# Kernel tuning notes

Hardware: AMD Instinct MI355X
Metric: run time of the kernel (lower is better)

## Reference

```python
import jax, jax.numpy as jnp
import numpy as np

N = 40000
E = 640000
D_IN = 128
D_HID = 128
N_CLS = 40


def setup_inputs() -> dict:
    key = jax.random.key(0)
    ks = jax.random.split(key, 12)
    x = jax.random.normal(ks[0], (N, D_IN), dtype=jnp.float32)
    edge_index = jax.random.randint(ks[1], (2, E), 0, N, dtype=jnp.int32)
    s = 1.0 / np.sqrt(D_IN)
    sh = 1.0 / np.sqrt(D_HID)
    sc = 1.0 / np.sqrt(4 * D_HID)
    # per-layer params: lin weight [out,in], combine weight [out, 4*out], bias [out]
    W0 = jax.random.uniform(ks[2], (D_HID, D_IN), jnp.float32, -s, s)
    C0 = jax.random.uniform(ks[3], (D_HID, 4 * D_HID), jnp.float32, -sc, sc)
    b0 = jnp.zeros((D_HID,), jnp.float32)
    W1 = jax.random.uniform(ks[4], (D_HID, D_HID), jnp.float32, -sh, sh)
    C1 = jax.random.uniform(ks[5], (D_HID, 4 * D_HID), jnp.float32, -sc, sc)
    b1 = jnp.zeros((D_HID,), jnp.float32)
    Wout = jax.random.uniform(ks[6], (N_CLS, D_HID), jnp.float32, -sh, sh)
    bout = jax.random.uniform(ks[7], (N_CLS,), jnp.float32, -sh, sh)
    return {"x": x, "edge_index": edge_index, "W0": W0, "C0": C0, "b0": b0,
            "W1": W1, "C1": C1, "b1": b1, "Wout": Wout, "bout": bout}


def _gcn_layer(x, row, col, W, C, b):
    n = x.shape[0]
    h = x @ W.T  # [N, H]
    ones = jnp.ones(row.shape, x.dtype)
    deg = jax.ops.segment_sum(ones, col, num_segments=n)  # in-degree incl. self-loops
    dinv = jnp.where(deg > 0, deg ** -0.5, 0.0)
    norm = dinv[row] * dinv[col]  # [E]
    msg = norm[:, None] * h[row]  # gather + scale, [E, H]
    add = jax.ops.segment_sum(msg, col, num_segments=n)
    mean = add / jnp.maximum(deg, 1.0)[:, None]
    mn = jax.ops.segment_min(msg, col, num_segments=n)
    mx = jax.ops.segment_max(msg, col, num_segments=n)
    out = jnp.concatenate([mean, add, mn, mx], axis=-1) @ C.T  # [N, H]
    return out + b


def reference(x, edge_index, W0, C0, b0, W1, C1, b1, Wout, bout):
    n = x.shape[0]
    loops = jnp.arange(n, dtype=edge_index.dtype)
    row = jnp.concatenate([edge_index[0], loops])
    col = jnp.concatenate([edge_index[1], loops])
    h = jax.nn.relu(_gcn_layer(x, row, col, W0, C0, b0))
    h = jax.nn.relu(_gcn_layer(h, row, col, W1, C1, b1))
    logits = h @ Wout.T + bout
    return jax.nn.log_softmax(logits, axis=-1)
```

## Files before the change

kernel.cpp:

```cpp
#include <hip/hip_runtime.h>
#include <hip/hip_fp16.h>
#include <math.h>

#define NN 40000
#define NE 640000
#define D 128
#define NCLS 40
#define CAP 64

typedef _Float16 f16x8 __attribute__((ext_vector_type(8)));
typedef float    f32x4 __attribute__((ext_vector_type(4)));

static inline int cdiv(int a, int b){ return (a + b - 1) / b; }

__global__ __launch_bounds__(256) void k_prep(int* __restrict__ cnt,
    const float* __restrict__ W0, _Float16* __restrict__ w0h,
    const float* __restrict__ C0, _Float16* __restrict__ c0h,
    const float* __restrict__ W1, _Float16* __restrict__ w1h,
    const float* __restrict__ C1, _Float16* __restrict__ c1h,
    const float* __restrict__ WO, _Float16* __restrict__ oh) {
  int i = blockIdx.x * 256 + threadIdx.x;
  if (i < NN) cnt[i] = 0;
  if (i < 16384) {
    float v = W0[i];
    int cc = i >> 7, k = i & 127;
    int pidx = (((cc >> 4) * 4 + (k >> 5)) * 64 + ((cc & 15) | (((k >> 3) & 3) << 4))) * 8 + (k & 7);
    w0h[pidx] = (_Float16)v;
  } else if (i < 81920) {
    int off = i - 16384;
    c0h[off] = (_Float16)C0[off];
  } else if (i < 98304) {
    int off = i - 81920;
    w1h[off] = (_Float16)W1[off];
  } else if (i < 163840) {
    int off = i - 98304;
    c1h[off] = (_Float16)C1[off];
  } else if (i < 168960) {
    int off = i - 163840;
    oh[off] = (_Float16)WO[off];
  }
}

__global__ __launch_bounds__(256) void k_fill(const int* __restrict__ row,
                                              const int* __restrict__ col,
                                              int* __restrict__ cnt,
                                              int* __restrict__ adj) {
  int i = blockIdx.x * 256 + threadIdx.x;
  if (i < NE) {
    int c = col[i];
    int s = atomicAdd(&cnt[c], 1);
    if (s < CAP) adj[c * CAP + s] = row[i];
  }
}

__global__ __launch_bounds__(256) void k_dinvlin(const int* __restrict__ cnt,
                                                 float* __restrict__ dinv,
                                                 const float* __restrict__ A,
                                                 const _Float16* __restrict__ Wh,
                                                 _Float16* __restrict__ out) {
  if (blockIdx.x < 157) {
    int i = blockIdx.x * 256 + threadIdx.x;
    if (i < NN) dinv[i] = rsqrtf((float)(cnt[i] + 1));
    return;
  }
  __shared__ f16x8 Ah[64 * 8];
  int t = threadIdx.x;
  int lane = t & 63, wid = t >> 6;
  int wr = wid >> 1, wc = wid & 1;
  int row0 = (blockIdx.x - 157) * 64;

  f32x4 acc[2][4];
  #pragma unroll
  for (int m = 0; m < 2; m++)
    #pragma unroll
    for (int n = 0; n < 4; n++) acc[m][n] = (f32x4){0.f, 0.f, 0.f, 0.f};

  for (int k0 = 0; k0 < 128; k0 += 64) {
    __syncthreads();
    #pragma unroll
    for (int c = 0; c < 2; c++) {
      int id = t + c * 256;
      int r = id >> 3, q = id & 7;
      int ch = r * 8 + (q ^ (r & 7));
      const float* src = &A[(size_t)(row0 + r) * 128 + k0 + q * 8];
      float4 v0 = *(const float4*)src;
      float4 v1 = *(const float4*)(src + 4);
      float vv[8] = {v0.x, v0.y, v0.z, v0.w, v1.x, v1.y, v1.z, v1.w};
      f16x8 hi;
      #pragma unroll
      for (int j = 0; j < 8; j++) hi[j] = (_Float16)vv[j];
      Ah[ch] = hi;
    }
    __syncthreads();
    #pragma unroll
    for (int ks = 0; ks < 2; ks++) {
      int kchunk = (k0 >> 5) + ks;
      f16x8 ah[2], bh[4];
      #pragma unroll
      for (int m = 0; m < 2; m++) {
        int row = wr * 32 + m * 16 + (lane & 15);
        int ch = row * 8 + ((ks * 4 + (lane >> 4)) ^ (row & 7));
        ah[m] = Ah[ch];
      }
      #pragma unroll
      for (int n = 0; n < 4; n++) {
        int fidx = (((wc * 4 + n) * 4 + kchunk) * 64 + lane) * 8;
        bh[n] = *(const f16x8*)&Wh[fidx];
      }
      #pragma unroll
      for (int m = 0; m < 2; m++)
        #pragma unroll
        for (int n = 0; n < 4; n++)
          acc[m][n] = __builtin_amdgcn_mfma_f32_16x16x32_f16(ah[m], bh[n], acc[m][n], 0, 0, 0);
    }
  }

  #pragma unroll
  for (int m = 0; m < 2; m++) {
    int rbase = row0 + wr * 32 + m * 16 + (lane >> 4) * 4;
    float rs[4];
    #pragma unroll
    for (int j = 0; j < 4; j++) rs[j] = rsqrtf((float)(cnt[rbase + j] + 1));
    #pragma unroll
    for (int n = 0; n < 4; n++) {
      int col = wc * 64 + n * 16 + (lane & 15);
      #pragma unroll
      for (int j = 0; j < 4; j++)
        out[(size_t)(rbase + j) * 128 + col] = (_Float16)(acc[m][n][j] * rs[j]);
    }
  }
}

__global__ __launch_bounds__(256) void k_agg(const _Float16* __restrict__ hs,
                                             const int* __restrict__ cnt,
                                             const int* __restrict__ adj,
                                             const float* __restrict__ dinv,
                                             _Float16* __restrict__ agg) {
  int t = threadIdx.x;
  int g = t >> 4;
  int sl = t & 15;
  int nd = blockIdx.x * 16 + g;
  float di = dinv[nd];
  f16x8 sum = *(const f16x8*)&hs[(size_t)nd * D + sl * 8];
  f16x8 mn = sum, mx = sum;
  int ec = cnt[nd]; if (ec > CAP) ec = CAP;
  const int* abase = &adj[(size_t)nd * CAP];

  for (int eb = 0; eb < ec; eb += 16) {
    int rem = ec - eb; if (rem > 16) rem = 16;
    int re = abase[eb + (sl < rem ? sl : rem - 1)];
    int j = 0;
    for (; j + 8 <= rem; j += 8) {
      int r[8]; f16x8 v[8];
      #pragma unroll
      for (int u = 0; u < 8; u++) r[u] = __shfl(re, j + u, 16);
      #pragma unroll
      for (int u = 0; u < 8; u++) v[u] = *(const f16x8*)&hs[(size_t)r[u] * D + sl * 8];
      #pragma unroll
      for (int u = 0; u < 8; u++) {
        sum += v[u];
        mn = __builtin_elementwise_min(mn, v[u]);
        mx = __builtin_elementwise_max(mx, v[u]);
      }
    }
    for (; j + 4 <= rem; j += 4) {
      int r[4]; f16x8 v[4];
      #pragma unroll
      for (int u = 0; u < 4; u++) r[u] = __shfl(re, j + u, 16);
      #pragma unroll
      for (int u = 0; u < 4; u++) v[u] = *(const f16x8*)&hs[(size_t)r[u] * D + sl * 8];
      #pragma unroll
      for (int u = 0; u < 4; u++) {
        sum += v[u];
        mn = __builtin_elementwise_min(mn, v[u]);
        mx = __builtin_elementwise_max(mx, v[u]);
      }
    }
    for (; j < rem; j++) {
      int r0 = __shfl(re, j, 16);
      f16x8 v0 = *(const f16x8*)&hs[(size_t)r0 * D + sl * 8];
      sum += v0;
      mn = __builtin_elementwise_min(mn, v0);
      mx = __builtin_elementwise_max(mx, v0);
    }
  }

  _Float16 dh = (_Float16)di;
  f16x8 dv = {dh, dh, dh, dh, dh, dh, dh, dh};
  size_t base = (size_t)nd * 384 + sl * 8;
  *(f16x8*)&agg[base +   0] = sum * dv;
  *(f16x8*)&agg[base + 128] = mn  * dv;
  *(f16x8*)&agg[base + 256] = mx  * dv;
}

template<int MODE>
__global__ __launch_bounds__(256, 4) void k_comb(const _Float16* __restrict__ agg,
                                                 const float* __restrict__ dinv,
                                                 const _Float16* __restrict__ CW,
                                                 const float* __restrict__ bias,
                                                 const _Float16* __restrict__ W2h,
                                                 const float* __restrict__ bias2,
                                                 void* __restrict__ outv) {
  __shared__ f16x8 As[32 * 48];
  __shared__ f16x8 Bs[128 * 8];
  int t = threadIdx.x;
  int lane = t & 63, wid = t >> 6;
  int nd0 = blockIdx.x * 32;

  #pragma unroll
  for (int c = 0; c < 6; c++) {
    int id = t + c * 256;
    int r = id / 48, q = id - r * 48;
    As[r * 48 + (q ^ (r & 7))] = *(const f16x8*)&agg[(size_t)(nd0 + r) * 384 + q * 8];
  }

  f32x4 accA[2][2], accM[2][2];
  #pragma unroll
  for (int m = 0; m < 2; m++)
    #pragma unroll
    for (int n = 0; n < 2; n++) {
      accA[m][n] = (f32x4){0.f, 0.f, 0.f, 0.f};
      accM[m][n] = (f32x4){0.f, 0.f, 0.f, 0.f};
    }

  for (int k0 = 0; k0 < 512; k0 += 64) {
    __syncthreads();
    #pragma unroll
    for (int c = 0; c < 4; c++) {
      int id = t + c * 256;
      int cc = id >> 3, kq = id & 7;
      Bs[cc * 8 + (kq ^ (cc & 7))] = *(const f16x8*)&CW[(size_t)cc * 512 + k0 + kq * 8];
    }
    __syncthreads();
    int qbase = ((k0 < 256) ? (k0 & 127) : (k0 - 128)) >> 3;
    bool isMean = (k0 < 128);
    #pragma unroll
    for (int ks = 0; ks < 2; ks++) {
      f16x8 a[2], b[2];
      #pragma unroll
      for (int m = 0; m < 2; m++) {
        int row = m * 16 + (lane & 15);
        int qq = qbase + ks * 4 + (lane >> 4);
        a[m] = As[row * 48 + (qq ^ (row & 7))];
      }
      #pragma unroll
      for (int n = 0; n < 2; n++) {
        int cc = wid * 32 + n * 16 + (lane & 15);
        b[n] = Bs[cc * 8 + ((ks * 4 + (lane >> 4)) ^ (cc & 7))];
      }
      #pragma unroll
      for (int m = 0; m < 2; m++)
        #pragma unroll
        for (int n = 0; n < 2; n++) {
          if (isMean)
            accM[m][n] = __builtin_amdgcn_mfma_f32_16x16x32_f16(a[m], b[n], accM[m][n], 0, 0, 0);
          else
            accA[m][n] = __builtin_amdgcn_mfma_f32_16x16x32_f16(a[m], b[n], accA[m][n], 0, 0, 0);
        }
    }
  }

  __syncthreads();
  _Float16* A2 = (_Float16*)As;
  #pragma unroll
  for (int m = 0; m < 2; m++) {
    int lr0 = m * 16 + (lane >> 4) * 4;
    float d2[4];
    #pragma unroll
    for (int j = 0; j < 4; j++) {
      float dvv = dinv[nd0 + lr0 + j];
      d2[j] = dvv * dvv;
    }
    #pragma unroll
    for (int n = 0; n < 2; n++) {
      int cc = wid * 32 + n * 16 + (lane & 15);
      float bv = bias[cc];
      #pragma unroll
      for (int j = 0; j < 4; j++) {
        float v = fmaxf(accA[m][n][j] + d2[j] * accM[m][n][j] + bv, 0.f);
        int r = lr0 + j;
        A2[(r * 48 + 32 + ((cc >> 3) ^ (r & 7))) * 8 + (cc & 7)] = (_Float16)v;
      }
    }
  }

  if constexpr (MODE == 0) {
    f32x4 acc2[2][2];
    #pragma unroll
    for (int m = 0; m < 2; m++)
      #pragma unroll
      for (int n = 0; n < 2; n++) acc2[m][n] = (f32x4){0.f, 0.f, 0.f, 0.f};
    for (int k0 = 0; k0 < 128; k0 += 64) {
      __syncthreads();
      #pragma unroll
      for (int c = 0; c < 4; c++) {
        int id = t + c * 256;
        int cc = id >> 3, kq = id & 7;
        Bs[cc * 8 + (kq ^ (cc & 7))] = *(const f16x8*)&W2h[(size_t)cc * 128 + k0 + kq * 8];
      }
      __syncthreads();
      #pragma unroll
      for (int ks = 0; ks < 2; ks++) {
        int qq = (k0 >> 3) + ks * 4 + (lane >> 4);
        f16x8 a[2], b[2];
        #pragma unroll
        for (int m = 0; m < 2; m++) {
          int row = m * 16 + (lane & 15);
          a[m] = As[row * 48 + 32 + (qq ^ (row & 7))];
        }
        #pragma unroll
        for (int n = 0; n < 2; n++) {
          int cc = wid * 32 + n * 16 + (lane & 15);
          b[n] = Bs[cc * 8 + ((ks * 4 + (lane >> 4)) ^ (cc & 7))];
        }
        #pragma unroll
        for (int m = 0; m < 2; m++)
          #pragma unroll
          for (int n = 0; n < 2; n++)
            acc2[m][n] = __builtin_amdgcn_mfma_f32_16x16x32_f16(a[m], b[n], acc2[m][n], 0, 0, 0);
      }
    }
    _Float16* out = (_Float16*)outv;
    #pragma unroll
    for (int m = 0; m < 2; m++) {
      int rbase = nd0 + m * 16 + (lane >> 4) * 4;
      float rs[4];
      #pragma unroll
      for (int j = 0; j < 4; j++) rs[j] = dinv[rbase + j];
      #pragma unroll
      for (int n = 0; n < 2; n++) {
        int cc = wid * 32 + n * 16 + (lane & 15);
        #pragma unroll
        for (int j = 0; j < 4; j++)
          out[(size_t)(rbase + j) * 128 + cc] = (_Float16)(acc2[m][n][j] * rs[j]);
      }
    }
  } else {
    f32x4 acc3[3];
    #pragma unroll
    for (int n = 0; n < 3; n++) acc3[n] = (f32x4){0.f, 0.f, 0.f, 0.f};
    __syncthreads();
    #pragma unroll
    for (int c = 0; c < 3; c++) {
      int id = t + c * 256;
      int r = id >> 4, q = id & 15;
      f16x8 hv = {};
      if (r < NCLS) hv = *(const f16x8*)&W2h[(size_t)r * 128 + q * 8];
      Bs[r * 16 + (q ^ (r & 15))] = hv;
    }
    __syncthreads();
    if (wid < 2) {
      #pragma unroll
      for (int ks = 0; ks < 4; ks++) {
        int arow = wid * 16 + (lane & 15);
        f16x8 a = As[arow * 48 + 32 + ((ks * 4 + (lane >> 4)) ^ (arow & 7))];
        #pragma unroll
        for (int n = 0; n < 3; n++) {
          int br = n * 16 + (lane & 15);
          f16x8 b = Bs[br * 16 + ((ks * 4 + (lane >> 4)) ^ (br & 15))];
          acc3[n] = __builtin_amdgcn_mfma_f32_16x16x32_f16(a, b, acc3[n], 0, 0, 0);
        }
      }
      float* out = (float*)outv;
      int cl = lane & 15;
      float bb[3];
      #pragma unroll
      for (int n = 0; n < 3; n++) {
        int c = n * 16 + cl;
        bb[n] = (c < NCLS) ? bias2[c] : 0.f;
      }
      #pragma unroll
      for (int j = 0; j < 4; j++) {
        float v[3];
        #pragma unroll
        for (int n = 0; n < 3; n++) {
          int c = n * 16 + cl;
          v[n] = (c < NCLS) ? acc3[n][j] + bb[n] : -INFINITY;
        }
        float m = fmaxf(fmaxf(v[0], v[1]), v[2]);
        #pragma unroll
        for (int off = 1; off < 16; off <<= 1) m = fmaxf(m, __shfl_xor(m, off, 16));
        float s = 0.f;
        #pragma unroll
        for (int n = 0; n < 3; n++) {
          int c = n * 16 + cl;
          if (c < NCLS) s += expf(v[n] - m);
        }
        #pragma unroll
        for (int off = 1; off < 16; off <<= 1) s += __shfl_xor(s, off, 16);
        float ls = logf(s);
        int row = nd0 + wid * 16 + (lane >> 4) * 4 + j;
        #pragma unroll
        for (int n = 0; n < 3; n++) {
          int c = n * 16 + cl;
          if (c < NCLS) out[(size_t)row * NCLS + c] = v[n] - m - ls;
        }
      }
    }
  }
}

extern "C" void kernel_launch(void* const* d_in, const int* in_sizes, int n_in,
                              void* d_out, int out_size, void* d_ws, size_t ws_size,
                              hipStream_t stream) {
  const float* x    = (const float*)d_in[0];
  const int*   ei   = (const int*)  d_in[1];
  const float* W0   = (const float*)d_in[2];
  const float* C0   = (const float*)d_in[3];
  const float* b0   = (const float*)d_in[4];
  const float* W1   = (const float*)d_in[5];
  const float* C1   = (const float*)d_in[6];
  const float* b1   = (const float*)d_in[7];
  const float* Wout = (const float*)d_in[8];
  const float* bout = (const float*)d_in[9];
  float* out = (float*)d_out;

  char* ws = (char*)d_ws;
  size_t o = 0;
  auto take = [&](size_t bytes) -> char* {
    char* p = ws + o;
    o += (bytes + 255) & ~(size_t)255;
    return p;
  };
  int*       cnt    = (int*)      take((size_t)NN * 4);
  int*       adj    = (int*)      take((size_t)NN * CAP * 4);
  float*     dinv   = (float*)    take((size_t)NN * 4);
  _Float16*  W0h    = (_Float16*) take(128 * 128 * 2);
  _Float16*  C0h    = (_Float16*) take(128 * 512 * 2);
  _Float16*  W1h    = (_Float16*) take(128 * 128 * 2);
  _Float16*  C1h    = (_Float16*) take(128 * 512 * 2);
  _Float16*  Oh     = (_Float16*) take(40 * 128 * 2);
  _Float16*  bufA   = (_Float16*) take((size_t)NN * 128 * 2);
  _Float16*  bufB   = (_Float16*) take((size_t)NN * 128 * 2);
  _Float16*  aggbuf = (_Float16*) take((size_t)NN * 384 * 2);

  const int* row = ei;
  const int* col = ei + NE;

  k_prep<<<cdiv(168960, 256), 256, 0, stream>>>(cnt, W0, W0h, C0, C0h,
                                                W1, W1h, C1, C1h, Wout, Oh);
  k_fill<<<cdiv(NE, 256), 256, 0, stream>>>(row, col, cnt, adj);
  k_dinvlin<<<157 + 625, 256, 0, stream>>>(cnt, dinv, x, W0h, bufA);
  k_agg<<<2500, 256, 0, stream>>>(bufA, cnt, adj, dinv, aggbuf);
  k_comb<0><<<1250, 256, 0, stream>>>(aggbuf, dinv, C0h, b0, W1h, nullptr, bufB);
  k_agg<<<2500, 256, 0, stream>>>(bufB, cnt, adj, dinv, aggbuf);
  k_comb<1><<<1250, 256, 0, stream>>>(aggbuf, dinv, C1h, b1, Oh, bout, out);
}
```

Measured before the change: 144.6 us.

## Fuse prep with edge fill, drop dinv buffer, widen combine tiles to 64 rows

Weight conversion and adjacency fill now run in one launch, and the count buffer is cleared with a memset instead of inside the prep kernel. The dinv array is gone: each kernel recomputes rsqrt from the counts where it needs it, which removes a pass over the nodes and a global buffer. The combine kernel now handles 64 nodes per block with more accumulators, so each weight tile is reused across more rows and all four waves take part in the output stage. The cost is more registers and shared memory per block, with occupancy lowered to 2 blocks and half as many blocks launched.

```diff
diff --git a/kernel.cpp b/kernel.cpp
--- a/kernel.cpp
+++ b/kernel.cpp
@@ -13,61 +13,53 @@
 
 static inline int cdiv(int a, int b){ return (a + b - 1) / b; }
 
-__global__ __launch_bounds__(256) void k_prep(int* __restrict__ cnt,
+__global__ __launch_bounds__(256) void k_prepfill(
     const float* __restrict__ W0, _Float16* __restrict__ w0h,
     const float* __restrict__ C0, _Float16* __restrict__ c0h,
     const float* __restrict__ W1, _Float16* __restrict__ w1h,
     const float* __restrict__ C1, _Float16* __restrict__ c1h,
-    const float* __restrict__ WO, _Float16* __restrict__ oh) {
-  int i = blockIdx.x * 256 + threadIdx.x;
-  if (i < NN) cnt[i] = 0;
-  if (i < 16384) {
-    float v = W0[i];
-    int cc = i >> 7, k = i & 127;
-    int pidx = (((cc >> 4) * 4 + (k >> 5)) * 64 + ((cc & 15) | (((k >> 3) & 3) << 4))) * 8 + (k & 7);
-    w0h[pidx] = (_Float16)v;
-  } else if (i < 81920) {
-    int off = i - 16384;
-    c0h[off] = (_Float16)C0[off];
-  } else if (i < 98304) {
-    int off = i - 81920;
-    w1h[off] = (_Float16)W1[off];
-  } else if (i < 163840) {
-    int off = i - 98304;
-    c1h[off] = (_Float16)C1[off];
-  } else if (i < 168960) {
-    int off = i - 163840;
-    oh[off] = (_Float16)WO[off];
+    const float* __restrict__ WO, _Float16* __restrict__ oh,
+    const int* __restrict__ row, const int* __restrict__ col,
+    int* __restrict__ cnt, int* __restrict__ adj) {
+  if (blockIdx.x < 660) {
+    int i = blockIdx.x * 256 + threadIdx.x;
+    if (i < 16384) {
+      float v = W0[i];
+      int cc = i >> 7, k = i & 127;
+      int pidx = (((cc >> 4) * 4 + (k >> 5)) * 64 + ((cc & 15) | (((k >> 3) & 3) << 4))) * 8 + (k & 7);
+      w0h[pidx] = (_Float16)v;
+    } else if (i < 81920) {
+      int off = i - 16384;
+      c0h[off] = (_Float16)C0[off];
+    } else if (i < 98304) {
+      int off = i - 81920;
+      w1h[off] = (_Float16)W1[off];
+    } else if (i < 163840) {
+      int off = i - 98304;
+      c1h[off] = (_Float16)C1[off];
+    } else if (i < 168960) {
+      int off = i - 163840;
+      oh[off] = (_Float16)WO[off];
+    }
+  } else {
+    int i = (blockIdx.x - 660) * 256 + threadIdx.x;
+    if (i < NE) {
+      int c = col[i];
+      int s = atomicAdd(&cnt[c], 1);
+      if (s < CAP) adj[c * CAP + s] = row[i];
+    }
   }
 }
 
-__global__ __launch_bounds__(256) void k_fill(const int* __restrict__ row,
-                                              const int* __restrict__ col,
-                                              int* __restrict__ cnt,
-                                              int* __restrict__ adj) {
-  int i = blockIdx.x * 256 + threadIdx.x;
-  if (i < NE) {
-    int c = col[i];
-    int s = atomicAdd(&cnt[c], 1);
-    if (s < CAP) adj[c * CAP + s] = row[i];
-  }
-}
-
-__global__ __launch_bounds__(256) void k_dinvlin(const int* __restrict__ cnt,
-                                                 float* __restrict__ dinv,
-                                                 const float* __restrict__ A,
-                                                 const _Float16* __restrict__ Wh,
-                                                 _Float16* __restrict__ out) {
-  if (blockIdx.x < 157) {
-    int i = blockIdx.x * 256 + threadIdx.x;
-    if (i < NN) dinv[i] = rsqrtf((float)(cnt[i] + 1));
-    return;
-  }
+__global__ __launch_bounds__(256) void k_lin(const int* __restrict__ cnt,
+                                             const float* __restrict__ A,
+                                             const _Float16* __restrict__ Wh,
+                                             _Float16* __restrict__ out) {
   __shared__ f16x8 Ah[64 * 8];
   int t = threadIdx.x;
   int lane = t & 63, wid = t >> 6;
   int wr = wid >> 1, wc = wid & 1;
-  int row0 = (blockIdx.x - 157) * 64;
+  int row0 = blockIdx.x * 64;
 
   f32x4 acc[2][4];
   #pragma unroll
@@ -134,16 +126,16 @@
 __global__ __launch_bounds__(256) void k_agg(const _Float16* __restrict__ hs,
                                              const int* __restrict__ cnt,
                                              const int* __restrict__ adj,
-                                             const float* __restrict__ dinv,
                                              _Float16* __restrict__ agg) {
   int t = threadIdx.x;
   int g = t >> 4;
   int sl = t & 15;
   int nd = blockIdx.x * 16 + g;
-  float di = dinv[nd];
+  int ec0 = cnt[nd];
+  float di = rsqrtf((float)(ec0 + 1));
   f16x8 sum = *(const f16x8*)&hs[(size_t)nd * D + sl * 8];
   f16x8 mn = sum, mx = sum;
-  int ec = cnt[nd]; if (ec > CAP) ec = CAP;
+  int ec = ec0 > CAP ? CAP : ec0;
   const int* abase = &adj[(size_t)nd * CAP];
 
   for (int eb = 0; eb < ec; eb += 16) {
@@ -194,29 +186,29 @@
 }
 
 template<int MODE>
-__global__ __launch_bounds__(256, 4) void k_comb(const _Float16* __restrict__ agg,
-                                                 const float* __restrict__ dinv,
+__global__ __launch_bounds__(256, 2) void k_comb(const _Float16* __restrict__ agg,
+                                                 const int* __restrict__ cnt,
                                                  const _Float16* __restrict__ CW,
                                                  const float* __restrict__ bias,
                                                  const _Float16* __restrict__ W2h,
                                                  const float* __restrict__ bias2,
                                                  void* __restrict__ outv) {
-  __shared__ f16x8 As[32 * 48];
+  __shared__ f16x8 As[64 * 48];
   __shared__ f16x8 Bs[128 * 8];
   int t = threadIdx.x;
   int lane = t & 63, wid = t >> 6;
-  int nd0 = blockIdx.x * 32;
+  int nd0 = blockIdx.x * 64;
 
   #pragma unroll
-  for (int c = 0; c < 6; c++) {
+  for (int c = 0; c < 12; c++) {
     int id = t + c * 256;
     int r = id / 48, q = id - r * 48;
     As[r * 48 + (q ^ (r & 7))] = *(const f16x8*)&agg[(size_t)(nd0 + r) * 384 + q * 8];
   }
 
-  f32x4 accA[2][2], accM[2][2];
+  f32x4 accA[4][2], accM[4][2];
   #pragma unroll
-  for (int m = 0; m < 2; m++)
+  for (int m = 0; m < 4; m++)
     #pragma unroll
     for (int n = 0; n < 2; n++) {
       accA[m][n] = (f32x4){0.f, 0.f, 0.f, 0.f};
@@ -236,9 +228,9 @@
     bool isMean = (k0 < 128);
     #pragma unroll
     for (int ks = 0; ks < 2; ks++) {
-      f16x8 a[2], b[2];
-      #pragma unroll
-      for (int m = 0; m < 2; m++) {
+      f16x8 a[4], b[2];
+      #pragma unroll
+      for (int m = 0; m < 4; m++) {
         int row = m * 16 + (lane & 15);
         int qq = qbase + ks * 4 + (lane >> 4);
         a[m] = As[row * 48 + (qq ^ (row & 7))];
@@ -249,7 +241,7 @@
         b[n] = Bs[cc * 8 + ((ks * 4 + (lane >> 4)) ^ (cc & 7))];
       }
       #pragma unroll
-      for (int m = 0; m < 2; m++)
+      for (int m = 0; m < 4; m++)
         #pragma unroll
         for (int n = 0; n < 2; n++) {
           if (isMean)
@@ -263,14 +255,12 @@
   __syncthreads();
   _Float16* A2 = (_Float16*)As;
   #pragma unroll
-  for (int m = 0; m < 2; m++) {
+  for (int m = 0; m < 4; m++) {
     int lr0 = m * 16 + (lane >> 4) * 4;
     float d2[4];
     #pragma unroll
-    for (int j = 0; j < 4; j++) {
-      float dvv = dinv[nd0 + lr0 + j];
-      d2[j] = dvv * dvv;
-    }
+    for (int j = 0; j < 4; j++)
+      d2[j] = 1.f / (float)(cnt[nd0 + lr0 + j] + 1);
     #pragma unroll
     for (int n = 0; n < 2; n++) {
       int cc = wid * 32 + n * 16 + (lane & 15);
@@ -285,9 +275,9 @@
   }
 
   if constexpr (MODE == 0) {
-    f32x4 acc2[2][2];
-    #pragma unroll
-    for (int m = 0; m < 2; m++)
+    f32x4 acc2[4][2];
+    #pragma unroll
+    for (int m = 0; m < 4; m++)
       #pragma unroll
       for (int n = 0; n < 2; n++) acc2[m][n] = (f32x4){0.f, 0.f, 0.f, 0.f};
     for (int k0 = 0; k0 < 128; k0 += 64) {
@@ -302,9 +292,9 @@
       #pragma unroll
       for (int ks = 0; ks < 2; ks++) {
         int qq = (k0 >> 3) + ks * 4 + (lane >> 4);
-        f16x8 a[2], b[2];
-        #pragma unroll
-        for (int m = 0; m < 2; m++) {
+        f16x8 a[4], b[2];
+        #pragma unroll
+        for (int m = 0; m < 4; m++) {
           int row = m * 16 + (lane & 15);
           a[m] = As[row * 48 + 32 + (qq ^ (row & 7))];
         }
@@ -314,7 +304,7 @@
           b[n] = Bs[cc * 8 + ((ks * 4 + (lane >> 4)) ^ (cc & 7))];
         }
         #pragma unroll
-        for (int m = 0; m < 2; m++)
+        for (int m = 0; m < 4; m++)
           #pragma unroll
           for (int n = 0; n < 2; n++)
             acc2[m][n] = __builtin_amdgcn_mfma_f32_16x16x32_f16(a[m], b[n], acc2[m][n], 0, 0, 0);
@@ -322,11 +312,11 @@
     }
     _Float16* out = (_Float16*)outv;
     #pragma unroll
-    for (int m = 0; m < 2; m++) {
+    for (int m = 0; m < 4; m++) {
       int rbase = nd0 + m * 16 + (lane >> 4) * 4;
       float rs[4];
       #pragma unroll
-      for (int j = 0; j < 4; j++) rs[j] = dinv[rbase + j];
+      for (int j = 0; j < 4; j++) rs[j] = rsqrtf((float)(cnt[rbase + j] + 1));
       #pragma unroll
       for (int n = 0; n < 2; n++) {
         int cc = wid * 32 + n * 16 + (lane & 15);
@@ -349,52 +339,50 @@
       Bs[r * 16 + (q ^ (r & 15))] = hv;
     }
     __syncthreads();
-    if (wid < 2) {
-      #pragma unroll
-      for (int ks = 0; ks < 4; ks++) {
-        int arow = wid * 16 + (lane & 15);
-        f16x8 a = As[arow * 48 + 32 + ((ks * 4 + (lane >> 4)) ^ (arow & 7))];
-        #pragma unroll
-        for (int n = 0; n < 3; n++) {
-          int br = n * 16 + (lane & 15);
-          f16x8 b = Bs[br * 16 + ((ks * 4 + (lane >> 4)) ^ (br & 15))];
-          acc3[n] = __builtin_amdgcn_mfma_f32_16x16x32_f16(a, b, acc3[n], 0, 0, 0);
-        }
-      }
-      float* out = (float*)outv;
-      int cl = lane & 15;
-      float bb[3];
+    #pragma unroll
+    for (int ks = 0; ks < 4; ks++) {
+      int arow = wid * 16 + (lane & 15);
+      f16x8 a = As[arow * 48 + 32 + ((ks * 4 + (lane >> 4)) ^ (arow & 7))];
+      #pragma unroll
+      for (int n = 0; n < 3; n++) {
+        int br = n * 16 + (lane & 15);
+        f16x8 b = Bs[br * 16 + ((ks * 4 + (lane >> 4)) ^ (br & 15))];
+        acc3[n] = __builtin_amdgcn_mfma_f32_16x16x32_f16(a, b, acc3[n], 0, 0, 0);
+      }
+    }
+    float* out = (float*)outv;
+    int cl = lane & 15;
+    float bb[3];
+    #pragma unroll
+    for (int n = 0; n < 3; n++) {
+      int c = n * 16 + cl;
+      bb[n] = (c < NCLS) ? bias2[c] : 0.f;
+    }
+    #pragma unroll
+    for (int j = 0; j < 4; j++) {
+      float v[3];
       #pragma unroll
       for (int n = 0; n < 3; n++) {
         int c = n * 16 + cl;
-        bb[n] = (c < NCLS) ? bias2[c] : 0.f;
-      }
-      #pragma unroll
-      for (int j = 0; j < 4; j++) {
-        float v[3];
-        #pragma unroll
-        for (int n = 0; n < 3; n++) {
-          int c = n * 16 + cl;
-          v[n] = (c < NCLS) ? acc3[n][j] + bb[n] : -INFINITY;
-        }
-        float m = fmaxf(fmaxf(v[0], v[1]), v[2]);
-        #pragma unroll
-        for (int off = 1; off < 16; off <<= 1) m = fmaxf(m, __shfl_xor(m, off, 16));
-        float s = 0.f;
-        #pragma unroll
-        for (int n = 0; n < 3; n++) {
-          int c = n * 16 + cl;
-          if (c < NCLS) s += expf(v[n] - m);
-        }
-        #pragma unroll
-        for (int off = 1; off < 16; off <<= 1) s += __shfl_xor(s, off, 16);
-        float ls = logf(s);
-        int row = nd0 + wid * 16 + (lane >> 4) * 4 + j;
-        #pragma unroll
-        for (int n = 0; n < 3; n++) {
-          int c = n * 16 + cl;
-          if (c < NCLS) out[(size_t)row * NCLS + c] = v[n] - m - ls;
-        }
+        v[n] = (c < NCLS) ? acc3[n][j] + bb[n] : -INFINITY;
+      }
+      float m = fmaxf(fmaxf(v[0], v[1]), v[2]);
+      #pragma unroll
+      for (int off = 1; off < 16; off <<= 1) m = fmaxf(m, __shfl_xor(m, off, 16));
+      float s = 0.f;
+      #pragma unroll
+      for (int n = 0; n < 3; n++) {
+        int c = n * 16 + cl;
+        if (c < NCLS) s += expf(v[n] - m);
+      }
+      #pragma unroll
+      for (int off = 1; off < 16; off <<= 1) s += __shfl_xor(s, off, 16);
+      float ls = logf(s);
+      int row = nd0 + wid * 16 + (lane >> 4) * 4 + j;
+      #pragma unroll
+      for (int n = 0; n < 3; n++) {
+        int c = n * 16 + cl;
+        if (c < NCLS) out[(size_t)row * NCLS + c] = v[n] - m - ls;
       }
     }
   }
@@ -424,7 +412,6 @@
   };
   int*       cnt    = (int*)      take((size_t)NN * 4);
   int*       adj    = (int*)      take((size_t)NN * CAP * 4);
-  float*     dinv   = (float*)    take((size_t)NN * 4);
   _Float16*  W0h    = (_Float16*) take(128 * 128 * 2);
   _Float16*  C0h    = (_Float16*) take(128 * 512 * 2);
   _Float16*  W1h    = (_Float16*) take(128 * 128 * 2);
@@ -437,12 +424,12 @@
   const int* row = ei;
   const int* col = ei + NE;
 
-  k_prep<<<cdiv(168960, 256), 256, 0, stream>>>(cnt, W0, W0h, C0, C0h,
-                                                W1, W1h, C1, C1h, Wout, Oh);
-  k_fill<<<cdiv(NE, 256), 256, 0, stream>>>(row, col, cnt, adj);
-  k_dinvlin<<<157 + 625, 256, 0, stream>>>(cnt, dinv, x, W0h, bufA);
-  k_agg<<<2500, 256, 0, stream>>>(bufA, cnt, adj, dinv, aggbuf);
-  k_comb<0><<<1250, 256, 0, stream>>>(aggbuf, dinv, C0h, b0, W1h, nullptr, bufB);
-  k_agg<<<2500, 256, 0, stream>>>(bufB, cnt, adj, dinv, aggbuf);
-  k_comb<1><<<1250, 256, 0, stream>>>(aggbuf, dinv, C1h, b1, Oh, bout, out);
+  hipMemsetAsync(cnt, 0, (size_t)NN * 4, stream);
+  k_prepfill<<<660 + 2500, 256, 0, stream>>>(W0, W0h, C0, C0h, W1, W1h, C1, C1h,
+                                             Wout, Oh, row, col, cnt, adj);
+  k_lin<<<625, 256, 0, stream>>>(cnt, x, W0h, bufA);
+  k_agg<<<2500, 256, 0, stream>>>(bufA, cnt, adj, aggbuf);
+  k_comb<0><<<625, 256, 0, stream>>>(aggbuf, cnt, C0h, b0, W1h, nullptr, bufB);
+  k_agg<<<2500, 256, 0, stream>>>(bufB, cnt, adj, aggbuf);
+  k_comb<1><<<625, 256, 0, stream>>>(aggbuf, cnt, C1h, b1, Oh, bout, out);
 }
```

Result: slower. 162.7 us (+12.6%).
